# Kernel optimization log

Hardware: AMD Instinct MI355X
Metric: run time of the kernel (lower is better)

## Reference

```python
import jax, jax.numpy as jnp
import numpy as np

NEG_SLOPE = 0.01  # nn.LeakyReLU default
N_NODES = 38332
POI_LEN = 38333
CAT_LEN = 400
POI_DIM = 300
CAT_DIM = 100
GCN_CH = 64
GCN_LAYERS = 5
N_EDGES = N_NODES * 32


def leaky(x):
    return jnp.where(x >= 0, x, NEG_SLOPE * x)


def gcn_conv(x, src, dst, W, b):
    """PyG GCNConv: add self loops + symmetric normalization.
    out = D^-1/2 (A+I) D^-1/2 X W + b, deg computed with self loops."""
    n = x.shape[0]
    h = x @ W  # [N, out]
    deg = jax.ops.segment_sum(jnp.ones_like(dst, dtype=h.dtype), dst, num_segments=n) + 1.0
    dinv = jax.lax.rsqrt(deg)  # deg >= 1 always (self loop)
    norm = dinv[src] * dinv[dst]  # [E]
    agg = jax.ops.segment_sum(h[src] * norm[:, None], dst, num_segments=n)
    agg = agg + h * (1.0 / deg)[:, None]  # self-loop term: norm_ii = 1/deg_i
    return agg + b


def setup_inputs() -> dict:
    key = jax.random.key(0)
    ks = jax.random.split(key, 16)
    poi_ids = jax.random.randint(ks[0], (N_NODES, 1), 0, POI_LEN).astype(jnp.float32)
    cat_ids = jax.random.randint(ks[1], (N_NODES, 1), 0, CAT_LEN).astype(jnp.float32)
    feats = jax.random.normal(ks[2], (N_NODES, 3), dtype=jnp.float32)
    x = jnp.concatenate([poi_ids, cat_ids, feats], axis=1)  # [N,5]
    edge_index = jax.random.randint(ks[3], (2, N_EDGES), 0, N_NODES, dtype=jnp.int32)

    def glorot(k, shape):
        lim = float(np.sqrt(6.0 / (shape[0] + shape[1])))
        return jax.random.uniform(k, shape, jnp.float32, -lim, lim)

    d_in = POI_DIM + CAT_DIM + 3  # 403
    params = {
        "poi_emb": jax.random.normal(ks[4], (POI_LEN, POI_DIM), jnp.float32),
        "cat_emb": jax.random.normal(ks[5], (CAT_LEN, CAT_DIM), jnp.float32),
        "W_in": glorot(ks[6], (d_in, GCN_CH)),
        "b_in": jnp.zeros((GCN_CH,), jnp.float32),
        "gcn_Ws": jnp.stack([glorot(jax.random.fold_in(ks[7], i), (GCN_CH, GCN_CH)) for i in range(GCN_LAYERS)]),
        "gcn_bs": jnp.zeros((GCN_LAYERS, GCN_CH), jnp.float32),
        "W_out": glorot(ks[8], (GCN_CH, 1)),
        "b_out": jnp.zeros((1,), jnp.float32),
        "fc1_W": glorot(ks[9], (N_NODES, 128)),
        "fc1_b": jnp.zeros((128,), jnp.float32),
        "fc2_W": glorot(ks[10], (128, POI_LEN)),
        "fc2_b": jnpos if False else jnp.zeros((POI_LEN,), jnp.float32),
    }
    return {"x": x, "edge_index": edge_index, **params}


def reference(x, edge_index, poi_emb, cat_emb, W_in, b_in, gcn_Ws, gcn_bs, W_out, b_out, fc1_W, fc1_b, fc2_W, fc2_b):
    src, dst = edge_index[0], edge_index[1]
    poi_f = poi_emb[x[:, 0].astype(jnp.int32)]  # [N,300]
    cat_f = cat_emb[x[:, 1].astype(jnp.int32)]  # [N,100]
    feat = jnp.concatenate([poi_f, cat_f, x[:, 2:5]], axis=1)  # [N,403]
    feat = leaky(gcn_conv(feat, src, dst, W_in, b_in))
    for i in range(GCN_LAYERS):
        t = gcn_conv(feat, src, dst, gcn_Ws[i], gcn_bs[i])
        feat = leaky(t) + t  # GcnUnit: relu(temp) + temp
    feat = leaky(gcn_conv(feat, src, dst, W_out, b_out)).reshape(-1)  # [N]
    h = jax.nn.relu(feat @ fc1_W + fc1_b)
    out = jax.nn.relu(h @ fc2_W + fc2_b)  # [poi_len]
    return out
```

## Files before the change

### kernel.cpp

```cpp
#include <hip/hip_runtime.h>
#include <hip/hip_bf16.h>

#define N_NODES 38332
#define POI_LEN 38333
#define CAT_LEN 400
#define POI_DIM 300
#define CAT_DIM 100
#define N_EDGES (N_NODES * 32)
#define NEG_SLOPE 0.01f
#define NSLOT 96

typedef __attribute__((ext_vector_type(8))) short short8;
typedef __attribute__((ext_vector_type(4))) float f32x4;

__device__ __forceinline__ unsigned short f2bf(float f) {
  unsigned u = __float_as_uint(f);
  u += 0x7fff + ((u >> 16) & 1);
  return (unsigned short)(u >> 16);
}
__device__ __forceinline__ float bflo(unsigned u) {
  return __uint_as_float(u << 16);
}
__device__ __forceinline__ float bfhi(unsigned u) {
  return __uint_as_float(u & 0xffff0000u);
}
__device__ __forceinline__ void acc8(float4& a0, float4& a1, uint4 v) {
  a0.x += bflo(v.x); a0.y += bfhi(v.x); a0.z += bflo(v.y); a0.w += bfhi(v.y);
  a1.x += bflo(v.z); a1.y += bfhi(v.z); a1.z += bflo(v.w); a1.w += bfhi(v.w);
}


#define WFIN_ELEMS (13 * 2048)
#define WFGCN_ELEMS (5 * 4096)

__global__ __launch_bounds__(256) void k_prep(const float* __restrict__ W_in,
                                              const float* __restrict__ gcn_Ws,
                                              unsigned short* __restrict__ wf_in,
                                              unsigned short* __restrict__ wf_gcn,
                                              int* __restrict__ cnt,
                                              float* __restrict__ h128) {
  int idx = blockIdx.x * 256 + threadIdx.x;
  if (idx < N_NODES) cnt[idx] = 0;
  if (idx < 128) h128[idx] = 0.f;
  if (idx < WFIN_ELEMS) {
    int j = idx & 7, n = (idx >> 3) & 63, q = (idx >> 9) & 3, ks = idx >> 11;
    int k = ks * 32 + q * 8 + j;
    wf_in[idx] = f2bf((k < 400) ? W_in[k * 64 + n] : 0.f);
  } else if (idx < WFIN_ELEMS + WFGCN_ELEMS) {
    int t = idx - WFIN_ELEMS;
    int l = t >> 12, i = t & 4095;
    int j = i & 7, n = (i >> 3) & 63, q = (i >> 9) & 3, ks = i >> 11;
    int k = ks * 32 + q * 8 + j;
    wf_gcn[t] = f2bf(gcn_Ws[(size_t)l * 4096 + k * 64 + n]);
  }
}


__global__ __launch_bounds__(256) void k_scatter(const int* __restrict__ src,
                                                 const int* __restrict__ dst,
                                                 int* __restrict__ cnt,
                                                 int* __restrict__ csr) {
  int i = blockIdx.x * 256 + threadIdx.x;
  if (i >= N_EDGES) return;
  int s = src[i];
  int d = dst[i];
  int pos = atomicAdd(&cnt[d], 1);
  csr[(size_t)d * NSLOT + pos] = s;
}


__global__ __launch_bounds__(256) void k_front(
    const float* __restrict__ x, const float* __restrict__ poi_emb,
    const float* __restrict__ cat_emb, const float* __restrict__ W_in,
    const unsigned short* __restrict__ wf_in, const int* __restrict__ cnt,
    float* __restrict__ dinv, unsigned short* __restrict__ hs) {
  constexpr int RS = 424;
  __shared__ unsigned short sA[16 * RS];
  __shared__ float sC[16 * 68];
  __shared__ int sPid[16], sCid[16];
  __shared__ float sX[16][3];
  __shared__ float sDinv[16];
  int tid = threadIdx.x;
  int row0 = blockIdx.x * 16;
  if (tid < 16) {
    int row = row0 + tid;
    if (row < N_NODES) {
      sPid[tid] = (int)x[row * 5 + 0];
      sCid[tid] = (int)x[row * 5 + 1];
      sX[tid][0] = x[row * 5 + 2];
      sX[tid][1] = x[row * 5 + 3];
      sX[tid][2] = x[row * 5 + 4];
      float dn = 1.0f / sqrtf((float)(cnt[row] + 1));
      sDinv[tid] = dn;
      dinv[row] = dn;
    } else {
      sPid[tid] = 0; sCid[tid] = 0;
      sX[tid][0] = sX[tid][1] = sX[tid][2] = 0.f;
      sDinv[tid] = 0.f;
    }
  }
  __syncthreads();
  for (int idx = tid; idx < 16 * 104; idx += 256) {
    int r = idx / 104;
    int k = (idx - r * 104) * 4;
    ushort4 o = {0, 0, 0, 0};
    if (k < 400 && row0 + r < N_NODES) {
      float4 f;
      if (k < 300) f = *(const float4*)(poi_emb + (size_t)sPid[r] * 300 + k);
      else         f = *(const float4*)(cat_emb + (size_t)sCid[r] * 100 + (k - 300));
      o.x = f2bf(f.x); o.y = f2bf(f.y); o.z = f2bf(f.z); o.w = f2bf(f.w);
    }
    *(ushort4*)&sA[r * RS + k] = o;
  }
  __syncthreads();
  int lane = tid & 63, wv = tid >> 6;
  int c = lane & 15, q = lane >> 4, n0 = wv * 16;
  f32x4 acc = {0.f, 0.f, 0.f, 0.f};
  const unsigned short* arow = &sA[c * RS];
#pragma unroll
  for (int ks = 0; ks < 13; ks++) {
    short8 af = *(const short8*)(arow + ks * 32 + q * 8);
    short8 bf = *(const short8*)(wf_in + ((size_t)((ks * 4 + q) * 64 + n0 + c)) * 8);
    acc = __builtin_amdgcn_mfma_f32_16x16x32_bf16(af, bf, acc, 0, 0, 0);
  }
#pragma unroll
  for (int r = 0; r < 4; r++) sC[(q * 4 + r) * 68 + n0 + c] = acc[r];
  __syncthreads();
  for (int idx = tid; idx < 16 * 64; idx += 256) {
    int r = idx >> 6, col = idx & 63;
    int row = row0 + r;
    if (row < N_NODES) {
      float v = sC[r * 68 + col] + sX[r][0] * W_in[400 * 64 + col] +
                sX[r][1] * W_in[401 * 64 + col] + sX[r][2] * W_in[402 * 64 + col];
      hs[(size_t)row * 64 + col] = f2bf(v * sDinv[r]);
    }
  }
}


template <int MODE>
__global__ __launch_bounds__(256) void k_agg(const unsigned short* __restrict__ hs,
                                             const int* __restrict__ cnt,
                                             const int* __restrict__ csr,
                                             const float* __restrict__ dinv,
                                             const float* __restrict__ bias,
                                             const unsigned short* __restrict__ Wf,
                                             unsigned short* __restrict__ hs_next,
                                             const float* __restrict__ W_out,
                                             float* __restrict__ hs1) {
  __shared__ unsigned short sA[16 * 72];
  __shared__ float sC[4 * 68];
  int tid = threadIdx.x;
  int lane = tid & 63;
  int wv = tid >> 6;
  int node = blockIdx.x * 4 + wv;
  int eslot = lane >> 3;
  int ch8 = lane & 7;
  if (MODE != 2) {
    for (int i = tid; i < 216; i += 256)
      *(ushort4*)&sA[288 + i * 4] = (ushort4){0, 0, 0, 0};
  }
  int deg = cnt[node];
  float dn = dinv[node];
  const int* crow = csr + (size_t)node * NSLOT;
  uint4 sv = {0, 0, 0, 0};
  if (lane < 8) sv = *(const uint4*)(hs + (size_t)node * 64 + ch8 * 8);
  float4 a0 = {0.f, 0.f, 0.f, 0.f}, a1 = a0;
  int j = eslot;
  for (; j + 24 < deg; j += 32) {
    int s0 = crow[j];
    int s1 = crow[j + 8];
    int s2 = crow[j + 16];
    int s3 = crow[j + 24];
    uint4 v0 = *(const uint4*)(hs + (size_t)s0 * 64 + ch8 * 8);
    uint4 v1 = *(const uint4*)(hs + (size_t)s1 * 64 + ch8 * 8);
    uint4 v2 = *(const uint4*)(hs + (size_t)s2 * 64 + ch8 * 8);
    uint4 v3 = *(const uint4*)(hs + (size_t)s3 * 64 + ch8 * 8);
    acc8(a0, a1, v0); acc8(a0, a1, v1); acc8(a0, a1, v2); acc8(a0, a1, v3);
  }
  if (j + 8 < deg) {
    int s0 = crow[j];
    int s1 = crow[j + 8];
    uint4 v0 = *(const uint4*)(hs + (size_t)s0 * 64 + ch8 * 8);
    uint4 v1 = *(const uint4*)(hs + (size_t)s1 * 64 + ch8 * 8);
    acc8(a0, a1, v0); acc8(a0, a1, v1);
    j += 16;
  }
  if (j < deg) {
    int s = crow[j];
    uint4 v = *(const uint4*)(hs + (size_t)s * 64 + ch8 * 8);
    acc8(a0, a1, v);
  }
#pragma unroll
  for (int off = 8; off <= 32; off <<= 1) {
    a0.x += __shfl_xor(a0.x, off, 64);
    a0.y += __shfl_xor(a0.y, off, 64);
    a0.z += __shfl_xor(a0.z, off, 64);
    a0.w += __shfl_xor(a0.w, off, 64);
    a1.x += __shfl_xor(a1.x, off, 64);
    a1.y += __shfl_xor(a1.y, off, 64);
    a1.z += __shfl_xor(a1.z, off, 64);
    a1.w += __shfl_xor(a1.w, off, 64);
  }
  if (lane < 8) {
    float4 bb0 = *(const float4*)(bias + ch8 * 8);
    float4 bb1 = *(const float4*)(bias + ch8 * 8 + 4);
    float4 t0, t1;
    t0.x = dn * (a0.x + bflo(sv.x)) + bb0.x;
    t0.y = dn * (a0.y + bfhi(sv.x)) + bb0.y;
    t0.z = dn * (a0.z + bflo(sv.y)) + bb0.z;
    t0.w = dn * (a0.w + bfhi(sv.y)) + bb0.w;
    t1.x = dn * (a1.x + bflo(sv.z)) + bb1.x;
    t1.y = dn * (a1.y + bfhi(sv.z)) + bb1.y;
    t1.z = dn * (a1.z + bflo(sv.w)) + bb1.z;
    t1.w = dn * (a1.w + bfhi(sv.w)) + bb1.w;
    float4 l0, l1, o0, o1;
    l0.x = (t0.x >= 0.f) ? t0.x : NEG_SLOPE * t0.x;
    l0.y = (t0.y >= 0.f) ? t0.y : NEG_SLOPE * t0.y;
    l0.z = (t0.z >= 0.f) ? t0.z : NEG_SLOPE * t0.z;
    l0.w = (t0.w >= 0.f) ? t0.w : NEG_SLOPE * t0.w;
    l1.x = (t1.x >= 0.f) ? t1.x : NEG_SLOPE * t1.x;
    l1.y = (t1.y >= 0.f) ? t1.y : NEG_SLOPE * t1.y;
    l1.z = (t1.z >= 0.f) ? t1.z : NEG_SLOPE * t1.z;
    l1.w = (t1.w >= 0.f) ? t1.w : NEG_SLOPE * t1.w;
    if (MODE == 0) {
      o0 = l0; o1 = l1;
    } else {
      o0.x = l0.x + t0.x; o0.y = l0.y + t0.y; o0.z = l0.z + t0.z; o0.w = l0.w + t0.w;
      o1.x = l1.x + t1.x; o1.y = l1.y + t1.y; o1.z = l1.z + t1.z; o1.w = l1.w + t1.w;
    }
    if (MODE == 2) {
      float4 w0 = *(const float4*)(W_out + ch8 * 8);
      float4 w1 = *(const float4*)(W_out + ch8 * 8 + 4);
      float p = o0.x * w0.x + o0.y * w0.y + o0.z * w0.z + o0.w * w0.w +
                o1.x * w1.x + o1.y * w1.y + o1.z * w1.z + o1.w * w1.w;
      p += __shfl_xor(p, 1, 64);
      p += __shfl_xor(p, 2, 64);
      p += __shfl_xor(p, 4, 64);
      if (lane == 0) hs1[node] = p * dn;
    } else {
      uint4 pk;
      pk.x = (unsigned)f2bf(o0.x) | ((unsigned)f2bf(o0.y) << 16);
      pk.y = (unsigned)f2bf(o0.z) | ((unsigned)f2bf(o0.w) << 16);
      pk.z = (unsigned)f2bf(o1.x) | ((unsigned)f2bf(o1.y) << 16);
      pk.w = (unsigned)f2bf(o1.z) | ((unsigned)f2bf(o1.w) << 16);
      *(uint4*)&sA[wv * 72 + ch8 * 8] = pk;
    }
  }
  if (MODE != 2) {
    __syncthreads();
    int c = lane & 15, q = lane >> 4, n0 = wv * 16;
    f32x4 acc = {0.f, 0.f, 0.f, 0.f};
    const unsigned short* arow = &sA[c * 72];
#pragma unroll
    for (int ks = 0; ks < 2; ks++) {
      short8 af = *(const short8*)(arow + ks * 32 + q * 8);
      short8 bf = *(const short8*)(Wf + ((size_t)((ks * 4 + q) * 64 + n0 + c)) * 8);
      acc = __builtin_amdgcn_mfma_f32_16x16x32_bf16(af, bf, acc, 0, 0, 0);
    }
    if (q == 0) {
#pragma unroll
      for (int r = 0; r < 4; r++) sC[r * 68 + n0 + c] = acc[r];
    }
    __syncthreads();
    if (tid < 128) {
      int r = tid >> 5, c2 = (tid & 31) * 2;
      int row = blockIdx.x * 4 + r;
      float dr = dinv[row];
      unsigned lo = f2bf(sC[r * 68 + c2] * dr);
      unsigned hi = f2bf(sC[r * 68 + c2 + 1] * dr);
      *(unsigned*)(hs_next + (size_t)row * 64 + c2) = lo | (hi << 16);
    }
  }
}


__global__ __launch_bounds__(256) void k_out_agg(const float* __restrict__ hs1,
                                                 const int* __restrict__ cnt,
                                                 const int* __restrict__ csr,
                                                 const float* __restrict__ dinv,
                                                 const float* __restrict__ b_out,
                                                 float* __restrict__ g) {
  int lane = threadIdx.x & 63;
  int w = threadIdx.x >> 6;
  int node = blockIdx.x * 4 + w;
  int deg = cnt[node];
  const int* crow = csr + (size_t)node * NSLOT;
  float acc = 0.f;
  for (int e = lane; e < deg; e += 64) acc += hs1[crow[e]];
#pragma unroll
  for (int off = 32; off; off >>= 1) acc += __shfl_xor(acc, off, 64);
  if (lane == 0) {
    float t = dinv[node] * (acc + hs1[node]) + b_out[0];
    g[node] = (t >= 0.f) ? t : NEG_SLOPE * t;
  }
}


__global__ __launch_bounds__(128) void k_fc1(const float* __restrict__ g,
                                             const float* __restrict__ fc1_W,
                                             float* __restrict__ h128) {
  int j = threadIdx.x;
  int base = blockIdx.x * 32;
  int end = base + 32;
  if (end > N_NODES) end = N_NODES;
  float acc = 0.f;
  int i = base;
  for (; i + 4 <= end; i += 4) {
    acc += g[i + 0] * fc1_W[(size_t)(i + 0) * 128 + j];
    acc += g[i + 1] * fc1_W[(size_t)(i + 1) * 128 + j];
    acc += g[i + 2] * fc1_W[(size_t)(i + 2) * 128 + j];
    acc += g[i + 3] * fc1_W[(size_t)(i + 3) * 128 + j];
  }
  for (; i < end; i++) acc += g[i] * fc1_W[(size_t)i * 128 + j];
  atomicAdd(&h128[j], acc);
}

__global__ __launch_bounds__(256) void k_fc2(const float* __restrict__ h128raw,
                                             const float* __restrict__ fc1_b,
                                             const float* __restrict__ fc2_W,
                                             const float* __restrict__ fc2_b,
                                             float* __restrict__ out) {
  __shared__ float sh[128];
  int tid = threadIdx.x;
  if (tid < 128) {
    float v = h128raw[tid] + fc1_b[tid];
    sh[tid] = (v > 0.f) ? v : 0.f;
  }
  __syncthreads();
  int p = blockIdx.x * 256 + tid;
  if (p < POI_LEN) {
    float acc = fc2_b[p];
#pragma unroll 8
    for (int j = 0; j < 128; j++) acc += sh[j] * fc2_W[(size_t)j * POI_LEN + p];
    out[p] = (acc > 0.f) ? acc : 0.f;
  }
}


extern "C" void kernel_launch(void* const* d_in, const int* in_sizes, int n_in,
                              void* d_out, int out_size, void* d_ws, size_t ws_size,
                              hipStream_t stream) {
  const float* x       = (const float*)d_in[0];
  const int*   ei      = (const int*)d_in[1];
  const float* poi_emb = (const float*)d_in[2];
  const float* cat_emb = (const float*)d_in[3];
  const float* W_in    = (const float*)d_in[4];
  const float* b_in    = (const float*)d_in[5];
  const float* gcn_Ws  = (const float*)d_in[6];
  const float* gcn_bs  = (const float*)d_in[7];
  const float* W_out   = (const float*)d_in[8];
  const float* b_out   = (const float*)d_in[9];
  const float* fc1_W   = (const float*)d_in[10];
  const float* fc1_b   = (const float*)d_in[11];
  const float* fc2_W   = (const float*)d_in[12];
  const float* fc2_b   = (const float*)d_in[13];
  const int* src = ei;
  const int* dst = ei + N_EDGES;

  char* p = (char*)d_ws;
  auto take = [&](size_t bytes) {
    char* r = p;
    p += (bytes + 255) & ~(size_t)255;
    return r;
  };
  int*   cnt  = (int*)take((size_t)N_NODES * 4);
  float* dinv = (float*)take((size_t)N_NODES * 4);
  int*   csr  = (int*)take((size_t)N_NODES * NSLOT * 4);
  unsigned short* hsA = (unsigned short*)take((size_t)N_NODES * 64 * 2);
  unsigned short* hsB = (unsigned short*)take((size_t)N_NODES * 64 * 2);
  float* hs1  = (float*)take((size_t)N_NODES * 4);
  float* g    = (float*)take((size_t)N_NODES * 4);
  float* h128 = (float*)take(128 * 4);
  unsigned short* wf_in  = (unsigned short*)take((size_t)WFIN_ELEMS * 2);
  unsigned short* wf_gcn = (unsigned short*)take((size_t)WFGCN_ELEMS * 2);
  float* out = (float*)d_out;

  const int nb4 = N_NODES / 4;
  const int nb16 = (N_NODES + 15) / 16;

  k_prep<<<(WFIN_ELEMS + WFGCN_ELEMS + 255) / 256, 256, 0, stream>>>(
      W_in, gcn_Ws, wf_in, wf_gcn, cnt, h128);
  k_scatter<<<(N_EDGES + 255) / 256, 256, 0, stream>>>(src, dst, cnt, csr);

  k_front<<<nb16, 256, 0, stream>>>(x, poi_emb, cat_emb, W_in, wf_in, cnt,
                                    dinv, hsA);

  k_agg<0><<<nb4, 256, 0, stream>>>(hsA, cnt, csr, dinv, b_in,
                                    wf_gcn + 0 * 4096, hsB, nullptr, nullptr);
  k_agg<1><<<nb4, 256, 0, stream>>>(hsB, cnt, csr, dinv, gcn_bs + 0 * 64,
                                    wf_gcn + 1 * 4096, hsA, nullptr, nullptr);
  k_agg<1><<<nb4, 256, 0, stream>>>(hsA, cnt, csr, dinv, gcn_bs + 1 * 64,
                                    wf_gcn + 2 * 4096, hsB, nullptr, nullptr);
  k_agg<1><<<nb4, 256, 0, stream>>>(hsB, cnt, csr, dinv, gcn_bs + 2 * 64,
                                    wf_gcn + 3 * 4096, hsA, nullptr, nullptr);
  k_agg<1><<<nb4, 256, 0, stream>>>(hsA, cnt, csr, dinv, gcn_bs + 3 * 64,
                                    wf_gcn + 4 * 4096, hsB, nullptr, nullptr);
  k_agg<2><<<nb4, 256, 0, stream>>>(hsB, cnt, csr, dinv, gcn_bs + 4 * 64,
                                    nullptr, nullptr, W_out, hs1);

  k_out_agg<<<nb4, 256, 0, stream>>>(hs1, cnt, csr, dinv, b_out, g);
  k_fc1<<<(N_NODES + 31) / 32, 128, 0, stream>>>(g, fc1_W, h128);
  k_fc2<<<(POI_LEN + 255) / 256, 256, 0, stream>>>(h128, fc1_b, fc2_W, fc2_b, out);
}
```

Measured before the change: 446.8 us.

## Build CSR via bucketed two-pass split/place and vectorize neighbor index loads

Replaces the per-edge global-atomic scatter into the padded CSR with a two-pass build. The first pass bins edges into 128-destination buckets using shared-memory histograms and one global atomic per bucket per block, writing packed (src, local dst) pairs to a staging area that reuses the hsA buffer. The second pass places each bucket's edges with shared-memory atomics and also computes cnt and dinv, so k_front now just reads dinv. The aggregation loop now loads four consecutive neighbor indices as one int4 per lane instead of strided scalar loads, at the cost of an extra kernel launch and staging traffic.

```diff
diff --git a/kernel.cpp b/kernel.cpp
--- a/kernel.cpp
+++ b/kernel.cpp
@@ -9,6 +9,10 @@
 #define N_EDGES (N_NODES * 32)
 #define NEG_SLOPE 0.01f
 #define NSLOT 96
+#define B1 ((N_NODES + 127) / 128)
+#define SPLIT_CHUNK 2048
+#define NSPLIT ((N_EDGES + SPLIT_CHUNK - 1) / SPLIT_CHUNK)
+#define BCAP 8192
 
 typedef __attribute__((ext_vector_type(8))) short short8;
 typedef __attribute__((ext_vector_type(4))) float f32x4;
@@ -37,10 +41,10 @@
                                               const float* __restrict__ gcn_Ws,
                                               unsigned short* __restrict__ wf_in,
                                               unsigned short* __restrict__ wf_gcn,
-                                              int* __restrict__ cnt,
+                                              int* __restrict__ bcnt,
                                               float* __restrict__ h128) {
   int idx = blockIdx.x * 256 + threadIdx.x;
-  if (idx < N_NODES) cnt[idx] = 0;
+  if (idx < B1) bcnt[idx] = 0;
   if (idx < 128) h128[idx] = 0.f;
   if (idx < WFIN_ELEMS) {
     int j = idx & 7, n = (idx >> 3) & 63, q = (idx >> 9) & 3, ks = idx >> 11;
@@ -56,24 +60,73 @@
 }
 
 
-__global__ __launch_bounds__(256) void k_scatter(const int* __restrict__ src,
-                                                 const int* __restrict__ dst,
-                                                 int* __restrict__ cnt,
-                                                 int* __restrict__ csr) {
-  int i = blockIdx.x * 256 + threadIdx.x;
-  if (i >= N_EDGES) return;
-  int s = src[i];
-  int d = dst[i];
-  int pos = atomicAdd(&cnt[d], 1);
-  csr[(size_t)d * NSLOT + pos] = s;
+__global__ __launch_bounds__(256) void k_split(const int* __restrict__ src,
+                                               const int* __restrict__ dst,
+                                               int* __restrict__ bcnt,
+                                               int* __restrict__ staging) {
+  __shared__ int hist[B1];
+  __shared__ int lbase[B1];
+  __shared__ int lcur[B1];
+  int tid = threadIdx.x;
+  int base = blockIdx.x * SPLIT_CHUNK;
+  int n = N_EDGES - base;
+  if (n > SPLIT_CHUNK) n = SPLIT_CHUNK;
+  for (int b = tid; b < B1; b += 256) {
+    hist[b] = 0;
+    lcur[b] = 0;
+  }
+  __syncthreads();
+  for (int i = tid; i < n; i += 256) atomicAdd(&hist[dst[base + i] >> 7], 1);
+  __syncthreads();
+  for (int b = tid; b < B1; b += 256) {
+    int c = hist[b];
+    lbase[b] = c ? atomicAdd(&bcnt[b], c) : 0;
+  }
+  __syncthreads();
+  for (int i = tid; i < n; i += 256) {
+    int d = dst[base + i];
+    int s = src[base + i];
+    int b = d >> 7;
+    int off = atomicAdd(&lcur[b], 1);
+    staging[(size_t)b * BCAP + lbase[b] + off] = (s << 7) | (d & 127);
+  }
+}
+
+__global__ __launch_bounds__(256) void k_place(const int* __restrict__ staging,
+                                               const int* __restrict__ bcnt,
+                                               int* __restrict__ csr,
+                                               int* __restrict__ cnt,
+                                               float* __restrict__ dinv) {
+  __shared__ int cur[128];
+  int b = blockIdx.x;
+  int tid = threadIdx.x;
+  int d0 = b * 128;
+  int nd = N_NODES - d0;
+  if (nd > 128) nd = 128;
+  int cnt_b = bcnt[b];
+  const int* st = staging + (size_t)b * BCAP;
+  if (tid < 128) cur[tid] = 0;
+  __syncthreads();
+  for (int i = tid; i < cnt_b; i += 256) {
+    int pk = st[i];
+    int dl = pk & 127;
+    int pos = atomicAdd(&cur[dl], 1);
+    csr[(size_t)(d0 + dl) * NSLOT + pos] = pk >> 7;
+  }
+  __syncthreads();
+  if (tid < nd) {
+    int v = cur[tid];
+    cnt[d0 + tid] = v;
+    dinv[d0 + tid] = 1.0f / sqrtf((float)(v + 1));
+  }
 }
 
 
 __global__ __launch_bounds__(256) void k_front(
     const float* __restrict__ x, const float* __restrict__ poi_emb,
     const float* __restrict__ cat_emb, const float* __restrict__ W_in,
-    const unsigned short* __restrict__ wf_in, const int* __restrict__ cnt,
-    float* __restrict__ dinv, unsigned short* __restrict__ hs) {
+    const unsigned short* __restrict__ wf_in, const float* __restrict__ dinv,
+    unsigned short* __restrict__ hs) {
   constexpr int RS = 424;
   __shared__ unsigned short sA[16 * RS];
   __shared__ float sC[16 * 68];
@@ -90,9 +143,7 @@
       sX[tid][0] = x[row * 5 + 2];
       sX[tid][1] = x[row * 5 + 3];
       sX[tid][2] = x[row * 5 + 4];
-      float dn = 1.0f / sqrtf((float)(cnt[row] + 1));
-      sDinv[tid] = dn;
-      dinv[row] = dn;
+      sDinv[tid] = dinv[row];
     } else {
       sPid[tid] = 0; sCid[tid] = 0;
       sX[tid][0] = sX[tid][1] = sX[tid][2] = 0.f;
@@ -166,30 +217,28 @@
   uint4 sv = {0, 0, 0, 0};
   if (lane < 8) sv = *(const uint4*)(hs + (size_t)node * 64 + ch8 * 8);
   float4 a0 = {0.f, 0.f, 0.f, 0.f}, a1 = a0;
-  int j = eslot;
-  for (; j + 24 < deg; j += 32) {
-    int s0 = crow[j];
-    int s1 = crow[j + 8];
-    int s2 = crow[j + 16];
-    int s3 = crow[j + 24];
-    uint4 v0 = *(const uint4*)(hs + (size_t)s0 * 64 + ch8 * 8);
-    uint4 v1 = *(const uint4*)(hs + (size_t)s1 * 64 + ch8 * 8);
-    uint4 v2 = *(const uint4*)(hs + (size_t)s2 * 64 + ch8 * 8);
-    uint4 v3 = *(const uint4*)(hs + (size_t)s3 * 64 + ch8 * 8);
-    acc8(a0, a1, v0); acc8(a0, a1, v1); acc8(a0, a1, v2); acc8(a0, a1, v3);
-  }
-  if (j + 8 < deg) {
-    int s0 = crow[j];
-    int s1 = crow[j + 8];
-    uint4 v0 = *(const uint4*)(hs + (size_t)s0 * 64 + ch8 * 8);
-    uint4 v1 = *(const uint4*)(hs + (size_t)s1 * 64 + ch8 * 8);
-    acc8(a0, a1, v0); acc8(a0, a1, v1);
-    j += 16;
-  }
-  if (j < deg) {
-    int s = crow[j];
-    uint4 v = *(const uint4*)(hs + (size_t)s * 64 + ch8 * 8);
-    acc8(a0, a1, v);
+  for (int j = eslot * 4; j < deg; j += 32) {
+    int4 s4 = *(const int4*)(crow + j);
+    if (j + 4 <= deg) {
+      uint4 v0 = *(const uint4*)(hs + (size_t)s4.x * 64 + ch8 * 8);
+      uint4 v1 = *(const uint4*)(hs + (size_t)s4.y * 64 + ch8 * 8);
+      uint4 v2 = *(const uint4*)(hs + (size_t)s4.z * 64 + ch8 * 8);
+      uint4 v3 = *(const uint4*)(hs + (size_t)s4.w * 64 + ch8 * 8);
+      acc8(a0, a1, v0); acc8(a0, a1, v1); acc8(a0, a1, v2); acc8(a0, a1, v3);
+    } else {
+      if (j + 1 <= deg) {
+        uint4 v = *(const uint4*)(hs + (size_t)s4.x * 64 + ch8 * 8);
+        acc8(a0, a1, v);
+      }
+      if (j + 2 <= deg) {
+        uint4 v = *(const uint4*)(hs + (size_t)s4.y * 64 + ch8 * 8);
+        acc8(a0, a1, v);
+      }
+      if (j + 3 <= deg) {
+        uint4 v = *(const uint4*)(hs + (size_t)s4.z * 64 + ch8 * 8);
+        acc8(a0, a1, v);
+      }
+    }
   }
 #pragma unroll
   for (int off = 8; off <= 32; off <<= 1) {
@@ -366,6 +415,7 @@
   };
   int*   cnt  = (int*)take((size_t)N_NODES * 4);
   float* dinv = (float*)take((size_t)N_NODES * 4);
+  int*   bcnt = (int*)take((size_t)B1 * 4);
   int*   csr  = (int*)take((size_t)N_NODES * NSLOT * 4);
   unsigned short* hsA = (unsigned short*)take((size_t)N_NODES * 64 * 2);
   unsigned short* hsB = (unsigned short*)take((size_t)N_NODES * 64 * 2);
@@ -374,17 +424,18 @@
   float* h128 = (float*)take(128 * 4);
   unsigned short* wf_in  = (unsigned short*)take((size_t)WFIN_ELEMS * 2);
   unsigned short* wf_gcn = (unsigned short*)take((size_t)WFGCN_ELEMS * 2);
+  int* staging = (int*)hsA;
   float* out = (float*)d_out;
 
   const int nb4 = N_NODES / 4;
   const int nb16 = (N_NODES + 15) / 16;
 
   k_prep<<<(WFIN_ELEMS + WFGCN_ELEMS + 255) / 256, 256, 0, stream>>>(
-      W_in, gcn_Ws, wf_in, wf_gcn, cnt, h128);
-  k_scatter<<<(N_EDGES + 255) / 256, 256, 0, stream>>>(src, dst, cnt, csr);
-
-  k_front<<<nb16, 256, 0, stream>>>(x, poi_emb, cat_emb, W_in, wf_in, cnt,
-                                    dinv, hsA);
+      W_in, gcn_Ws, wf_in, wf_gcn, bcnt, h128);
+  k_split<<<NSPLIT, 256, 0, stream>>>(src, dst, bcnt, staging);
+  k_place<<<B1, 256, 0, stream>>>(staging, bcnt, csr, cnt, dinv);
+
+  k_front<<<nb16, 256, 0, stream>>>(x, poi_emb, cat_emb, W_in, wf_in, dinv, hsA);
 
   k_agg<0><<<nb4, 256, 0, stream>>>(hsA, cnt, csr, dinv, b_in,
                                     wf_gcn + 0 * 4096, hsB, nullptr, nullptr);
```

After: 414.6 us. 7.2% less time.
